# Performance work log

Hardware: AMD Instinct MI355X
Metric: run time of the kernel (lower is better)

The kernel has to match this reference:

```python
import jax, jax.numpy as jnp
import numpy as np

D_MODEL = 768
N_HEADS = 12
HEAD_DIM = D_MODEL // N_HEADS


def setup_inputs() -> dict:
    key = jax.random.key(0)
    ks = jax.random.split(key, 9)
    s = 1.0 / np.sqrt(D_MODEL)
    return {
        "x": jax.random.normal(ks[0], (2, 2048, D_MODEL), dtype=jnp.float32),
        "Wq": jax.random.uniform(ks[1], (D_MODEL, D_MODEL), minval=-s, maxval=s, dtype=jnp.float32),
        "bq": jax.random.uniform(ks[2], (D_MODEL,), minval=-s, maxval=s, dtype=jnp.float32),
        "Wk": jax.random.uniform(ks[3], (D_MODEL, D_MODEL), minval=-s, maxval=s, dtype=jnp.float32),
        "bk": jax.random.uniform(ks[4], (D_MODEL,), minval=-s, maxval=s, dtype=jnp.float32),
        "Wv": jax.random.uniform(ks[5], (D_MODEL, D_MODEL), minval=-s, maxval=s, dtype=jnp.float32),
        "bv": jax.random.uniform(ks[6], (D_MODEL,), minval=-s, maxval=s, dtype=jnp.float32),
        "Wo": jax.random.uniform(ks[7], (D_MODEL, D_MODEL), minval=-s, maxval=s, dtype=jnp.float32),
        "bo": jax.random.uniform(ks[8], (D_MODEL,), minval=-s, maxval=s, dtype=jnp.float32),
    }


def reference(x, Wq, bq, Wk, bk, Wv, bv, Wo, bo):
    B, S, D = x.shape
    H, Hd = N_HEADS, HEAD_DIM
    # nn.Linear: y = x @ W.T + b
    q = (x @ Wq.T + bq).reshape(B, S, H, Hd).transpose(0, 2, 1, 3)  # [B,H,S,Hd]
    k = (x @ Wk.T + bk).reshape(B, S, H, Hd).transpose(0, 2, 1, 3)
    v = (x @ Wv.T + bv).reshape(B, S, H, Hd).transpose(0, 2, 1, 3)
    scores = jnp.einsum('bhqd,bhkd->bhqk', q, k) / np.sqrt(Hd)  # [B,H,S,S]
    attn = jax.nn.softmax(scores, axis=-1)
    out = jnp.einsum('bhqk,bhkd->bhqd', attn, v)  # [B,H,S,Hd]
    out = out.transpose(0, 2, 1, 3).reshape(B, S, D)
    return out @ Wo.T + bo
```

## Files before the change

### kernel.cpp

```cpp
#include <hip/hip_runtime.h>

#define D_MODEL 768
#define SEQ 2048
#define BATCH 2
#define NHEADS 12
#define HDIM 64
#define M_TOTAL (BATCH*SEQ)
#define NQK (2*D_MODEL)

typedef __attribute__((ext_vector_type(8))) short short8;
typedef __attribute__((ext_vector_type(4))) short short4_t;
typedef __attribute__((ext_vector_type(4))) float floatx4;

#define EXP2(x) __builtin_amdgcn_exp2f(x)

static __device__ __forceinline__ unsigned short f2bf(float f) {
    union { float f; unsigned int u; } v; v.f = f;
    unsigned int r = (v.u + 0x7fffu + ((v.u >> 16) & 1u)) >> 16;
    return (unsigned short)r;
}

static __device__ __forceinline__ void async16(void* lds, const void* g) {
    __builtin_amdgcn_global_load_lds(
        (const __attribute__((address_space(1))) unsigned int*)g,
        (__attribute__((address_space(3))) unsigned int*)lds, 16, 0, 0);
}

#define X8    393216
#define W8    73728
#define CVT_N (X8 + 4*W8)
#define CVT_BLOCKS (CVT_N/256 + 6)
__global__ __launch_bounds__(256) void cvt_all_kernel(
    const float* __restrict__ x,  const float* __restrict__ Wq,
    const float* __restrict__ Wk, const float* __restrict__ Wv,
    const float* __restrict__ Wo, const float* __restrict__ bq,
    const float* __restrict__ bk,
    unsigned short* __restrict__ xb, unsigned short* __restrict__ wqk,
    unsigned short* __restrict__ wvb, unsigned short* __restrict__ wob,
    float* __restrict__ bqk)
{
    int i = blockIdx.x * 256 + threadIdx.x;
    if (i >= CVT_N) {
        int j = i - CVT_N;
        if (j < 1536) bqk[j] = (j < 768) ? bq[j] : bk[j - 768];
        return;
    }
    const float* src; unsigned short* dst;
    if (i < X8)             { src = x  + (size_t)i*8;            dst = xb  + (size_t)i*8; }
    else if (i < X8 + W8)   { int j = i - X8;          src = Wq + (size_t)j*8; dst = wqk + (size_t)j*8; }
    else if (i < X8 + 2*W8) { int j = i - (X8 + W8);   src = Wk + (size_t)j*8; dst = wqk + 589824 + (size_t)j*8; }
    else if (i < X8 + 3*W8) { int j = i - (X8 + 2*W8); src = Wv + (size_t)j*8; dst = wvb + (size_t)j*8; }
    else                    { int j = i - (X8 + 3*W8); src = Wo + (size_t)j*8; dst = wob + (size_t)j*8; }
    const float4* s = (const float4*)src;
    float4 a = s[0], b = s[1];
    short8 o;
    o[0]=(short)f2bf(a.x); o[1]=(short)f2bf(a.y); o[2]=(short)f2bf(a.z); o[3]=(short)f2bf(a.w);
    o[4]=(short)f2bf(b.x); o[5]=(short)f2bf(b.y); o[6]=(short)f2bf(b.z); o[7]=(short)f2bf(b.w);
    *(short8*)dst = o;
}

template<int MI, int NI>
__device__ __forceinline__ void gemm_core32(
    const unsigned short* __restrict__ A, const unsigned short* __restrict__ W,
    int m0, int n0, unsigned short* smem, floatx4 (&acc)[MI][NI], int t)
{
    const int ASZ = MI*32*32;
    const int WSZ = NI*32*32;
    const int BSZ = ASZ + WSZ;
    const int quad = (t >> 4) & 3, l = t & 15;
    const int wvv = t >> 6, wr = wvv >> 1, wc = wvv & 1;
    const int base_off = t & ~63;

    auto stage = [&](int buf, int kt) {
        char* AsB = (char*)(smem + buf*BSZ);
        char* WsB = (char*)(smem + buf*BSZ + ASZ);
#pragma unroll
        for (int it = 0; it < (MI+1)/2; ++it) {
            int slot = it*256 + t;
            if (slot < MI*128) {
                int r = slot >> 2, c = (slot & 3) ^ ((r >> 1) & 3);
                async16(AsB + (size_t)(it*256 + base_off)*16, A + (size_t)(m0+r)*768 + kt*32 + c*8);
            }
        }
#pragma unroll
        for (int it = 0; it < (NI+1)/2; ++it) {
            int slot = it*256 + t;
            if (slot < NI*128) {
                int r = slot >> 2, c = (slot & 3) ^ ((r >> 1) & 3);
                async16(WsB + (size_t)(it*256 + base_off)*16, W + (size_t)(n0+r)*768 + kt*32 + c*8);
            }
        }
    };

    stage(0, 0);
    for (int kt = 0; kt < 24; ++kt) {
        __syncthreads();
        if (kt < 23) stage((kt+1)&1, kt+1);
        const char* AsB = (const char*)(smem + (kt&1)*BSZ);
        const char* WsB = (const char*)(smem + (kt&1)*BSZ + ASZ);
        short8 af[MI], wf[NI];
#pragma unroll
        for (int mi = 0; mi < MI; ++mi) {
            int m = wr*(MI*16) + mi*16 + l;
            af[mi] = *(const short8*)(AsB + m*64 + ((quad ^ ((m>>1)&3))*16));
        }
#pragma unroll
        for (int ni = 0; ni < NI; ++ni) {
            int n = wc*(NI*16) + ni*16 + l;
            wf[ni] = *(const short8*)(WsB + n*64 + ((quad ^ ((n>>1)&3))*16));
        }
#pragma unroll
        for (int mi = 0; mi < MI; ++mi)
#pragma unroll
            for (int ni = 0; ni < NI; ++ni)
                acc[mi][ni] = __builtin_amdgcn_mfma_f32_16x16x32_bf16(
                    af[mi], wf[ni], acc[mi][ni], 0, 0, 0);
    }
}

__global__ __launch_bounds__(256, 3) void gemm_qkvt_kernel(
    const unsigned short* __restrict__ xb, const unsigned short* __restrict__ wqk,
    const unsigned short* __restrict__ wvb,
    const float* __restrict__ bqk, const float* __restrict__ bv,
    unsigned short* __restrict__ qkout, unsigned short* __restrict__ vtout)
{
    __shared__ unsigned short smem[14336];
    const int t = threadIdx.x;
    const int bid = blockIdx.x;
    const int lane = t & 63, quad = lane >> 4, l = lane & 15;
    const int wvv = t >> 6, wc = wvv & 1, wr = wvv >> 1;

    if (bid < 512) {
        int m0 = (bid >> 4)*128, n0 = (bid & 15)*96;
        floatx4 acc[4][3];
#pragma unroll
        for (int i=0;i<4;i++)
#pragma unroll
            for (int j=0;j<3;j++) acc[i][j] = (floatx4){0.f,0.f,0.f,0.f};
        gemm_core32<4,3>(xb, wqk, m0, n0, smem, acc, t);

        __syncthreads();
#pragma unroll
        for (int mi=0;mi<4;mi++)
#pragma unroll
            for (int ni=0;ni<3;ni++) {
                int col = wc*48 + ni*16 + l;
                float bcol = bqk[n0 + col];
#pragma unroll
                for (int r=0;r<4;r++) {
                    int row = wr*64 + mi*16 + quad*4 + r;
                    smem[row*96 + col] = f2bf(acc[mi][ni][r] + bcol);
                }
            }
        __syncthreads();
#pragma unroll
        for (int i=0;i<6;i++) {
            int slot = i*256 + t;
            int r = slot/12, c = slot - r*12;
            short8 val = *(const short8*)(smem + r*96 + c*8);
            *(short8*)(qkout + (size_t)(m0+r)*NQK + n0 + c*8) = val;
        }
    } else {
        int v = bid - 512;
        int m0 = (v & 7)*96, n0 = (v >> 3)*128;
        floatx4 acc[3][4];
#pragma unroll
        for (int i=0;i<3;i++)
#pragma unroll
            for (int j=0;j<4;j++) acc[i][j] = (floatx4){0.f,0.f,0.f,0.f};
        gemm_core32<3,4>(wvb, xb, m0, n0, smem, acc, t);

        __syncthreads();
#pragma unroll
        for (int mi=0;mi<3;mi++)
#pragma unroll
            for (int ni=0;ni<4;ni++) {
                int col = wc*64 + ni*16 + l;
#pragma unroll
                for (int r=0;r<4;r++) {
                    int row = wr*48 + mi*16 + quad*4 + r;
                    smem[row*128 + col] = f2bf(acc[mi][ni][r] + bv[m0 + row]);
                }
            }
        __syncthreads();
#pragma unroll
        for (int i=0;i<6;i++) {
            int slot = i*256 + t;
            int r = slot >> 4, c = slot & 15;
            int kb32 = (c >> 2)*32 + (c & 3)*4;
            short4_t lo = *(const short4_t*)(smem + r*128 + kb32);
            short4_t hi = *(const short4_t*)(smem + r*128 + kb32 + 16);
            short8 val;
            val[0]=lo[0]; val[1]=lo[1]; val[2]=lo[2]; val[3]=lo[3];
            val[4]=hi[0]; val[5]=hi[1]; val[6]=hi[2]; val[7]=hi[3];
            int f = m0 + r, tok = n0 + c*8;
            *(short8*)(vtout + ((size_t)(tok>>11)*768 + f)*SEQ + (tok & (SEQ-1))) = val;
        }
    }
}

__global__ __launch_bounds__(256, 3) void gemm_out_kernel(
    const unsigned short* __restrict__ ab, const unsigned short* __restrict__ wob,
    const float* __restrict__ bo, float* __restrict__ out)
{
    __shared__ unsigned short smem[8192];
    const int t = threadIdx.x;
    int bid = blockIdx.x;
    int m0 = (bid/12)*64, n0 = (bid%12)*64;

    floatx4 acc[2][2];
#pragma unroll
    for (int i=0;i<2;i++)
#pragma unroll
        for (int j=0;j<2;j++) acc[i][j] = (floatx4){0.f,0.f,0.f,0.f};

    gemm_core32<2,2>(ab, wob, m0, n0, smem, acc, t);

    const int lane = t & 63, quad = lane >> 4, l = lane & 15;
    const int wvv = t >> 6, wr = wvv >> 1, wc = wvv & 1;
#pragma unroll
    for (int mi=0;mi<2;mi++)
#pragma unroll
        for (int ni=0;ni<2;ni++) {
            int col = n0 + wc*32 + ni*16 + l;
            float bb = bo[col];
#pragma unroll
            for (int r=0;r<4;r++) {
                int row = m0 + wr*32 + mi*16 + quad*4 + r;
                out[(size_t)row*768 + col] = acc[mi][ni][r] + bb;
            }
        }
}

__global__ __launch_bounds__(256) void attn_kernel(
    const unsigned short* __restrict__ qk,
    const unsigned short* __restrict__ vt,
    unsigned short* __restrict__ aout)
{
    __shared__ unsigned short Ks[128*64];
    __shared__ unsigned short Vs[64*128];
    char* KsB = (char*)Ks; char* VsB = (char*)Vs;
    const int t = threadIdx.x;
    const int lane = t & 63, w = t >> 6;
    const int l16 = lane & 15, quad = lane >> 4;
    const int h = blockIdx.x;
    const int q0 = blockIdx.y * 64;
    const int b = blockIdx.z;
    const size_t rowbase = (size_t)b * SEQ;
    const size_t vbase = ((size_t)(b*NHEADS + h))*HDIM*SEQ;
    const int base_off = t & ~63;

    short8 qf0, qf1;
    {
        const unsigned short* qr = qk + (rowbase + q0 + w*16 + l16)*NQK + h*64;
        qf0 = *(const short8*)(qr + quad*8);
        qf1 = *(const short8*)(qr + 32 + quad*8);
    }

    floatx4 oacc[4];
#pragma unroll
    for (int i=0;i<4;i++) oacc[i] = (floatx4){0.f,0.f,0.f,0.f};
    float lsum = 0.f;
    short4_t pf[8];

    const float C1 = 0.18033688011112042f;
    const float C2 = -4.32808512266689f;

    for (int kt = 0; kt < SEQ/128; ++kt) {
        __syncthreads();
#pragma unroll
        for (int it = 0; it < 4; ++it) {
            int slot = it*256 + t;
            int r = slot >> 3, c = (slot & 7) ^ (r & 7);
            async16(KsB + (size_t)(it*256 + base_off)*16,
                    qk + (rowbase + kt*128 + r)*NQK + 768 + h*64 + c*8);
        }
#pragma unroll
        for (int it = 0; it < 4; ++it) {
            int slot = it*256 + t;
            int d = slot >> 4, c = (slot & 15) ^ (d & 15);
            async16(VsB + (size_t)(it*256 + base_off)*16,
                    vt + vbase + (size_t)d*SEQ + kt*128 + c*8);
        }
        __syncthreads();

#pragma unroll
        for (int mt = 0; mt < 8; ++mt) {
            int key = mt*16 + l16;
            short8 kf0 = *(const short8*)(KsB + key*128 + ((quad     ^ (l16&7))*16));
            short8 kf1 = *(const short8*)(KsB + key*128 + (((4+quad) ^ (l16&7))*16));
            floatx4 s = (floatx4){0.f,0.f,0.f,0.f};
            s = __builtin_amdgcn_mfma_f32_16x16x32_bf16(kf0, qf0, s, 0, 0, 0);
            s = __builtin_amdgcn_mfma_f32_16x16x32_bf16(kf1, qf1, s, 0, 0, 0);
            float p0 = EXP2(fmaf(s[0], C1, C2));
            float p1 = EXP2(fmaf(s[1], C1, C2));
            float p2 = EXP2(fmaf(s[2], C1, C2));
            float p3 = EXP2(fmaf(s[3], C1, C2));
            lsum += (p0 + p1) + (p2 + p3);
            short4_t pk;
            pk[0] = (short)f2bf(p0); pk[1] = (short)f2bf(p1);
            pk[2] = (short)f2bf(p2); pk[3] = (short)f2bf(p3);
            pf[mt] = pk;
        }

#pragma unroll
        for (int P = 0; P < 4; ++P) {
            short8 pcomb = __builtin_shufflevector(pf[2*P], pf[2*P+1],
                                                   0, 1, 2, 3, 4, 5, 6, 7);
#pragma unroll
            for (int ni = 0; ni < 4; ++ni) {
                int row = ni*16 + l16;
                short8 vv = *(const short8*)(VsB + row*256 + (((P*4 + quad) ^ l16)*16));
                oacc[ni] = __builtin_amdgcn_mfma_f32_16x16x32_bf16(pcomb, vv, oacc[ni], 0, 0, 0);
            }
        }
    }

    lsum += __shfl_xor(lsum, 16);
    lsum += __shfl_xor(lsum, 32);
    float inv[4];
#pragma unroll
    for (int r = 0; r < 4; ++r)
        inv[r] = 1.0f / __shfl(lsum, quad*4 + r);

    __syncthreads();
    unsigned short* Ob = Ks;
#pragma unroll
    for (int ni = 0; ni < 4; ++ni)
#pragma unroll
        for (int r = 0; r < 4; ++r) {
            int row = w*16 + quad*4 + r;
            Ob[row*72 + ni*16 + l16] = f2bf(oacc[ni][r] * inv[r]);
        }
    __syncthreads();
#pragma unroll
    for (int it = 0; it < 2; ++it) {
        int slot = it*256 + t;
        int r = slot >> 3, c = slot & 7;
        *(short8*)(aout + (rowbase + q0 + r)*768 + h*64 + c*8) = *(const short8*)(Ob + r*72 + c*8);
    }
}

extern "C" void kernel_launch(void* const* d_in, const int* in_sizes, int n_in,
                              void* d_out, int out_size, void* d_ws, size_t ws_size,
                              hipStream_t stream)
{
    const float* x  = (const float*)d_in[0];
    const float* Wq = (const float*)d_in[1];
    const float* bq = (const float*)d_in[2];
    const float* Wk = (const float*)d_in[3];
    const float* bk = (const float*)d_in[4];
    const float* Wv = (const float*)d_in[5];
    const float* bv = (const float*)d_in[6];
    const float* Wo = (const float*)d_in[7];
    const float* bo = (const float*)d_in[8];

    unsigned short* ws = (unsigned short*)d_ws;
    unsigned short* xb  = ws;
    unsigned short* wqk = xb  + (size_t)3145728;
    unsigned short* wvb = wqk + (size_t)1179648;
    unsigned short* wob = wvb + (size_t)589824;
    unsigned short* qkb = wob + (size_t)589824;
    unsigned short* vtb = qkb + (size_t)6291456;
    unsigned short* ab  = vtb + (size_t)3145728;
    float* bqk = (float*)(ab + (size_t)3145728);

    cvt_all_kernel<<<CVT_BLOCKS, 256, 0, stream>>>(x, Wq, Wk, Wv, Wo, bq, bk,
                                                   xb, wqk, wvb, wob, bqk);

    gemm_qkvt_kernel<<<768, 256, 0, stream>>>(xb, wqk, wvb, bqk, bv, qkb, vtb);

    attn_kernel<<<dim3(NHEADS, SEQ/64, BATCH), 256, 0, stream>>>(qkb, vtb, ab);

    gemm_out_kernel<<<768, 256, 0, stream>>>(ab, wob, bo, (float*)d_out);
}
```

Measured before the change: 165.7 us.

## Fuse fp32-to-bf16 conversion into GEMM loaders and drop the separate convert kernel

Removes the standalone conversion kernel that wrote bf16 copies of x and all weights. The GEMMs now read fp32 directly into registers, convert to bf16, and write to shared memory after the MFMA step, which overlaps the global loads with compute. This saves one launch and a full read/write pass over the converted data. In exchange, the GEMMs read twice as many bytes per tile, repeat the conversion in every block that reuses a tile, and need more registers, which may lower occupancy.

```diff
diff --git a/kernel.cpp b/kernel.cpp
--- a/kernel.cpp
+++ b/kernel.cpp
@@ -26,76 +26,117 @@
         (__attribute__((address_space(3))) unsigned int*)lds, 16, 0, 0);
 }
 
-#define X8    393216
-#define W8    73728
-#define CVT_N (X8 + 4*W8)
-#define CVT_BLOCKS (CVT_N/256 + 6)
-__global__ __launch_bounds__(256) void cvt_all_kernel(
-    const float* __restrict__ x,  const float* __restrict__ Wq,
-    const float* __restrict__ Wk, const float* __restrict__ Wv,
-    const float* __restrict__ Wo, const float* __restrict__ bq,
-    const float* __restrict__ bk,
-    unsigned short* __restrict__ xb, unsigned short* __restrict__ wqk,
-    unsigned short* __restrict__ wvb, unsigned short* __restrict__ wob,
-    float* __restrict__ bqk)
+template<int MI, int NI, bool AF32, bool WF32>
+__device__ __forceinline__ void gemm_core(
+    const void* Ap, const void* Wp, int m0, int n0,
+    unsigned short* smem, floatx4 (&acc)[MI][NI], int t)
 {
-    int i = blockIdx.x * 256 + threadIdx.x;
-    if (i >= CVT_N) {
-        int j = i - CVT_N;
-        if (j < 1536) bqk[j] = (j < 768) ? bq[j] : bk[j - 768];
-        return;
-    }
-    const float* src; unsigned short* dst;
-    if (i < X8)             { src = x  + (size_t)i*8;            dst = xb  + (size_t)i*8; }
-    else if (i < X8 + W8)   { int j = i - X8;          src = Wq + (size_t)j*8; dst = wqk + (size_t)j*8; }
-    else if (i < X8 + 2*W8) { int j = i - (X8 + W8);   src = Wk + (size_t)j*8; dst = wqk + 589824 + (size_t)j*8; }
-    else if (i < X8 + 3*W8) { int j = i - (X8 + 2*W8); src = Wv + (size_t)j*8; dst = wvb + (size_t)j*8; }
-    else                    { int j = i - (X8 + 3*W8); src = Wo + (size_t)j*8; dst = wob + (size_t)j*8; }
-    const float4* s = (const float4*)src;
-    float4 a = s[0], b = s[1];
-    short8 o;
-    o[0]=(short)f2bf(a.x); o[1]=(short)f2bf(a.y); o[2]=(short)f2bf(a.z); o[3]=(short)f2bf(a.w);
-    o[4]=(short)f2bf(b.x); o[5]=(short)f2bf(b.y); o[6]=(short)f2bf(b.z); o[7]=(short)f2bf(b.w);
-    *(short8*)dst = o;
-}
-
-template<int MI, int NI>
-__device__ __forceinline__ void gemm_core32(
-    const unsigned short* __restrict__ A, const unsigned short* __restrict__ W,
-    int m0, int n0, unsigned short* smem, floatx4 (&acc)[MI][NI], int t)
-{
-    const int ASZ = MI*32*32;
-    const int WSZ = NI*32*32;
-    const int BSZ = ASZ + WSZ;
+    const int ASZ = MI*1024;
+    const int BSZ = ASZ + NI*1024;
     const int quad = (t >> 4) & 3, l = t & 15;
     const int wvv = t >> 6, wr = wvv >> 1, wc = wvv & 1;
     const int base_off = t & ~63;
-
-    auto stage = [&](int buf, int kt) {
-        char* AsB = (char*)(smem + buf*BSZ);
-        char* WsB = (char*)(smem + buf*BSZ + ASZ);
-#pragma unroll
-        for (int it = 0; it < (MI+1)/2; ++it) {
-            int slot = it*256 + t;
-            if (slot < MI*128) {
-                int r = slot >> 2, c = (slot & 3) ^ ((r >> 1) & 3);
-                async16(AsB + (size_t)(it*256 + base_off)*16, A + (size_t)(m0+r)*768 + kt*32 + c*8);
-            }
-        }
-#pragma unroll
-        for (int it = 0; it < (NI+1)/2; ++it) {
-            int slot = it*256 + t;
-            if (slot < NI*128) {
-                int r = slot >> 2, c = (slot & 3) ^ ((r >> 1) & 3);
-                async16(WsB + (size_t)(it*256 + base_off)*16, W + (size_t)(n0+r)*768 + kt*32 + c*8);
+    const int AIT = (MI+1)/2, WIT = (NI+1)/2;
+
+    float4 areg[AIT][2];
+    float4 wreg[WIT][2];
+
+    auto loads = [&](int kt) {
+        if (AF32) {
+            const float* A = (const float*)Ap;
+#pragma unroll
+            for (int it = 0; it < AIT; ++it) {
+                int slot = it*256 + t;
+                if (slot < MI*128) {
+                    int r = slot >> 2, c = (slot & 3) ^ ((r >> 1) & 3);
+                    const float* p = A + (size_t)(m0+r)*768 + kt*32 + c*8;
+                    areg[it][0] = *(const float4*)p;
+                    areg[it][1] = *(const float4*)(p + 4);
+                }
+            }
+        }
+        if (WF32) {
+            const float* W = (const float*)Wp;
+#pragma unroll
+            for (int it = 0; it < WIT; ++it) {
+                int slot = it*256 + t;
+                if (slot < NI*128) {
+                    int r = slot >> 2, c = (slot & 3) ^ ((r >> 1) & 3);
+                    const float* p = W + (size_t)(n0+r)*768 + kt*32 + c*8;
+                    wreg[it][0] = *(const float4*)p;
+                    wreg[it][1] = *(const float4*)(p + 4);
+                }
             }
         }
     };
-
-    stage(0, 0);
+    auto asyncs = [&](int buf, int kt) {
+        if (!AF32) {
+            const unsigned short* A = (const unsigned short*)Ap;
+            char* AsB = (char*)(smem + buf*BSZ);
+#pragma unroll
+            for (int it = 0; it < AIT; ++it) {
+                int slot = it*256 + t;
+                if (slot < MI*128) {
+                    int r = slot >> 2, c = (slot & 3) ^ ((r >> 1) & 3);
+                    async16(AsB + (size_t)(it*256 + base_off)*16,
+                            A + (size_t)(m0+r)*768 + kt*32 + c*8);
+                }
+            }
+        }
+        if (!WF32) {
+            const unsigned short* W = (const unsigned short*)Wp;
+            char* WsB = (char*)(smem + buf*BSZ + ASZ);
+#pragma unroll
+            for (int it = 0; it < WIT; ++it) {
+                int slot = it*256 + t;
+                if (slot < NI*128) {
+                    int r = slot >> 2, c = (slot & 3) ^ ((r >> 1) & 3);
+                    async16(WsB + (size_t)(it*256 + base_off)*16,
+                            W + (size_t)(n0+r)*768 + kt*32 + c*8);
+                }
+            }
+        }
+    };
+    auto writes = [&](int buf) {
+        if (AF32) {
+            unsigned short* As = smem + buf*BSZ;
+#pragma unroll
+            for (int it = 0; it < AIT; ++it) {
+                int slot = it*256 + t;
+                if (slot < MI*128) {
+                    float4 a = areg[it][0], b = areg[it][1];
+                    short8 o;
+                    o[0]=(short)f2bf(a.x); o[1]=(short)f2bf(a.y);
+                    o[2]=(short)f2bf(a.z); o[3]=(short)f2bf(a.w);
+                    o[4]=(short)f2bf(b.x); o[5]=(short)f2bf(b.y);
+                    o[6]=(short)f2bf(b.z); o[7]=(short)f2bf(b.w);
+                    *(short8*)(As + (size_t)slot*8) = o;
+                }
+            }
+        }
+        if (WF32) {
+            unsigned short* Ws = smem + buf*BSZ + ASZ;
+#pragma unroll
+            for (int it = 0; it < WIT; ++it) {
+                int slot = it*256 + t;
+                if (slot < NI*128) {
+                    float4 a = wreg[it][0], b = wreg[it][1];
+                    short8 o;
+                    o[0]=(short)f2bf(a.x); o[1]=(short)f2bf(a.y);
+                    o[2]=(short)f2bf(a.z); o[3]=(short)f2bf(a.w);
+                    o[4]=(short)f2bf(b.x); o[5]=(short)f2bf(b.y);
+                    o[6]=(short)f2bf(b.z); o[7]=(short)f2bf(b.w);
+                    *(short8*)(Ws + (size_t)slot*8) = o;
+                }
+            }
+        }
+    };
+
+    asyncs(0, 0); loads(0); writes(0);
+
     for (int kt = 0; kt < 24; ++kt) {
         __syncthreads();
-        if (kt < 23) stage((kt+1)&1, kt+1);
+        if (kt < 23) { asyncs((kt+1)&1, kt+1); loads(kt+1); }
         const char* AsB = (const char*)(smem + (kt&1)*BSZ);
         const char* WsB = (const char*)(smem + (kt&1)*BSZ + ASZ);
         short8 af[MI], wf[NI];
@@ -115,29 +156,33 @@
             for (int ni = 0; ni < NI; ++ni)
                 acc[mi][ni] = __builtin_amdgcn_mfma_f32_16x16x32_bf16(
                     af[mi], wf[ni], acc[mi][ni], 0, 0, 0);
+        if (kt < 23) writes((kt+1)&1);
     }
 }
 
 __global__ __launch_bounds__(256, 3) void gemm_qkvt_kernel(
-    const unsigned short* __restrict__ xb, const unsigned short* __restrict__ wqk,
-    const unsigned short* __restrict__ wvb,
-    const float* __restrict__ bqk, const float* __restrict__ bv,
+    const float* __restrict__ x,  const float* __restrict__ Wq,
+    const float* __restrict__ Wk, const float* __restrict__ Wv,
+    const float* __restrict__ bq, const float* __restrict__ bk,
+    const float* __restrict__ bv,
     unsigned short* __restrict__ qkout, unsigned short* __restrict__ vtout)
 {
     __shared__ unsigned short smem[14336];
     const int t = threadIdx.x;
     const int bid = blockIdx.x;
-    const int lane = t & 63, quad = lane >> 4, l = lane & 15;
+    const int quad = (t >> 4) & 3, l = t & 15;
     const int wvv = t >> 6, wc = wvv & 1, wr = wvv >> 1;
 
     if (bid < 512) {
         int m0 = (bid >> 4)*128, n0 = (bid & 15)*96;
+        const float* Wsrc = (n0 < 768) ? Wq : Wk;
+        int nn0 = (n0 < 768) ? n0 : n0 - 768;
         floatx4 acc[4][3];
 #pragma unroll
         for (int i=0;i<4;i++)
 #pragma unroll
             for (int j=0;j<3;j++) acc[i][j] = (floatx4){0.f,0.f,0.f,0.f};
-        gemm_core32<4,3>(xb, wqk, m0, n0, smem, acc, t);
+        gemm_core<4,3,true,true>(x, Wsrc, m0, nn0, smem, acc, t);
 
         __syncthreads();
 #pragma unroll
@@ -145,7 +190,8 @@
 #pragma unroll
             for (int ni=0;ni<3;ni++) {
                 int col = wc*48 + ni*16 + l;
-                float bcol = bqk[n0 + col];
+                int gn = n0 + col;
+                float bcol = (n0 < 768) ? bq[gn] : bk[gn - 768];
 #pragma unroll
                 for (int r=0;r<4;r++) {
                     int row = wr*64 + mi*16 + quad*4 + r;
@@ -168,7 +214,7 @@
         for (int i=0;i<3;i++)
 #pragma unroll
             for (int j=0;j<4;j++) acc[i][j] = (floatx4){0.f,0.f,0.f,0.f};
-        gemm_core32<3,4>(wvb, xb, m0, n0, smem, acc, t);
+        gemm_core<3,4,true,true>(Wv, x, m0, n0, smem, acc, t);
 
         __syncthreads();
 #pragma unroll
@@ -200,7 +246,7 @@
 }
 
 __global__ __launch_bounds__(256, 3) void gemm_out_kernel(
-    const unsigned short* __restrict__ ab, const unsigned short* __restrict__ wob,
+    const unsigned short* __restrict__ ab, const float* __restrict__ Wo,
     const float* __restrict__ bo, float* __restrict__ out)
 {
     __shared__ unsigned short smem[8192];
@@ -214,9 +260,9 @@
 #pragma unroll
         for (int j=0;j<2;j++) acc[i][j] = (floatx4){0.f,0.f,0.f,0.f};
 
-    gemm_core32<2,2>(ab, wob, m0, n0, smem, acc, t);
-
-    const int lane = t & 63, quad = lane >> 4, l = lane & 15;
+    gemm_core<2,2,false,true>(ab, Wo, m0, n0, smem, acc, t);
+
+    const int quad = (t >> 4) & 3, l = t & 15;
     const int wvv = t >> 6, wr = wvv >> 1, wc = wvv & 1;
 #pragma unroll
     for (int mi=0;mi<2;mi++)
@@ -241,8 +287,8 @@
     __shared__ unsigned short Vs[64*128];
     char* KsB = (char*)Ks; char* VsB = (char*)Vs;
     const int t = threadIdx.x;
-    const int lane = t & 63, w = t >> 6;
-    const int l16 = lane & 15, quad = lane >> 4;
+    const int w = t >> 6;
+    const int l16 = t & 15, quad = (t >> 4) & 3;
     const int h = blockIdx.x;
     const int q0 = blockIdx.y * 64;
     const int b = blockIdx.z;
@@ -356,21 +402,13 @@
     const float* bo = (const float*)d_in[8];
 
     unsigned short* ws = (unsigned short*)d_ws;
-    unsigned short* xb  = ws;
-    unsigned short* wqk = xb  + (size_t)3145728;
-    unsigned short* wvb = wqk + (size_t)1179648;
-    unsigned short* wob = wvb + (size_t)589824;
-    unsigned short* qkb = wob + (size_t)589824;
+    unsigned short* qkb = ws;
     unsigned short* vtb = qkb + (size_t)6291456;
     unsigned short* ab  = vtb + (size_t)3145728;
-    float* bqk = (float*)(ab + (size_t)3145728);
-
-    cvt_all_kernel<<<CVT_BLOCKS, 256, 0, stream>>>(x, Wq, Wk, Wv, Wo, bq, bk,
-                                                   xb, wqk, wvb, wob, bqk);
-
-    gemm_qkvt_kernel<<<768, 256, 0, stream>>>(xb, wqk, wvb, bqk, bv, qkb, vtb);
+
+    gemm_qkvt_kernel<<<768, 256, 0, stream>>>(x, Wq, Wk, Wv, bq, bk, bv, qkb, vtb);
 
     attn_kernel<<<dim3(NHEADS, SEQ/64, BATCH), 256, 0, stream>>>(qkb, vtb, ab);
 
-    gemm_out_kernel<<<768, 256, 0, stream>>>(ab, wob, bo, (float*)d_out);
-}
+    gemm_out_kernel<<<768, 256, 0, stream>>>(ab, Wo, bo, (float*)d_out);
+}
```

Result: slower. 183.1 us (+10.5%).
